# Kernel tuning notes

Measured on AMD Instinct MI355X. Metric: run time of the kernel, lower is better.

The kernel has to match this reference:

```python
import jax, jax.numpy as jnp
import numpy as np

DIM = 2048
NUM_SLOTS = 64
MEM_DIM = 512
TEMP = 0.1


def setup_inputs() -> dict:
    key = jax.random.key(0)
    k_x, k_mem, k_kp, k_vp, k_gw, k_gb = jax.random.split(key, 6)
    B, L = 8, 4096
    return {
        "x": jax.random.normal(k_x, (B, L, DIM), dtype=jnp.float32),
        "memory": jax.random.normal(k_mem, (NUM_SLOTS, MEM_DIM), dtype=jnp.float32),
        # torch Linear weight layout: [out_features, in_features]
        "key_w": jax.random.normal(k_kp, (MEM_DIM, DIM), dtype=jnp.float32) * (1.0 / np.sqrt(DIM)),
        "value_w": jax.random.normal(k_vp, (DIM, MEM_DIM), dtype=jnp.float32) * (1.0 / np.sqrt(MEM_DIM)),
        "gate_w": jax.random.normal(k_gw, (1, 2 * DIM), dtype=jnp.float32) * (1.0 / np.sqrt(2 * DIM)),
        "gate_b": jnp.zeros((1,), dtype=jnp.float32),
    }


def reference(x, memory, key_w, value_w, gate_w, gate_b):
    # query = key_proj(x): [B,L,mem_dim]
    query = jnp.einsum('bld,md->blm', x, key_w)
    # attention over memory slots: [B,L,num_slots]
    attn = jax.nn.softmax(jnp.einsum('blm,nm->bln', query, memory) / TEMP, axis=-1)
    # retrieve and project back to dim: [B,L,dim]
    retrieved = jnp.einsum('bln,nm->blm', attn, memory)
    retrieved = jnp.einsum('blm,dm->bld', retrieved, value_w)
    # gate from concat([x, retrieved]) -> Linear(2*dim, 1) -> sigmoid
    gate_logit = (jnp.einsum('bld,od->blo', x, gate_w[:, :DIM])
                  + jnp.einsum('bld,od->blo', retrieved, gate_w[:, DIM:])
                  + gate_b)
    gate = jax.nn.sigmoid(gate_logit)  # [B,L,1]
    return gate * x + (1.0 - gate) * retrieved
```

## Files before the change

kernel.cpp:

```cpp
#include <hip/hip_runtime.h>
#include <stdint.h>

#define DIM   2048
#define NSLOT 64
#define MDIM  512
#define TINV  10.0f

typedef __attribute__((ext_vector_type(4))) float     f32x4;
typedef __attribute__((ext_vector_type(8))) _Float16  half8;
typedef __attribute__((ext_vector_type(4))) unsigned int u32x4;

#define MFMA16(a,b,c) __builtin_amdgcn_mfma_f32_16x16x32_f16((a),(b),(c),0,0,0)

#define OFF_W2H   0
#define OFF_W2L   327680
#define OFF_W3T   655360
#define OFF_H     917504
#define OFF_TPART 917760


__global__ __launch_bounds__(256) void prep_w2(
    const float* __restrict__ memory, const float* __restrict__ key_w,
    const float* __restrict__ gate_w, _Float16* __restrict__ W2h,
    _Float16* __restrict__ W2l)
{
    const int tid = threadIdx.x;
    const int c = blockIdx.x;
    const int g = blockIdx.y;
    const int k = c * 256 + tid;

    if (g == 8) {
        float v = gate_w[k];
        _Float16 ph = (_Float16)v;
        _Float16 pl = (_Float16)(v - (float)ph);
        W2h[(size_t)64 * DIM + k] = ph;
        W2l[(size_t)64 * DIM + k] = pl;
        for (int r = 65; r < 80; ++r) {
            W2h[(size_t)r * DIM + k] = (_Float16)0.f;
            W2l[(size_t)r * DIM + k] = (_Float16)0.f;
        }
        return;
    }

    __shared__ __align__(16) float mem_s[8 * MDIM];
    for (int i = tid; i < 8 * MDIM; i += 256)
        mem_s[i] = memory[g * 8 * MDIM + i];
    __syncthreads();

    const f32x4* ms4 = (const f32x4*)mem_s;
    float acc[8] = {};
    for (int m4 = 0; m4 < MDIM / 4; ++m4) {
        const float kw0 = key_w[(size_t)(m4 * 4 + 0) * DIM + k];
        const float kw1 = key_w[(size_t)(m4 * 4 + 1) * DIM + k];
        const float kw2 = key_w[(size_t)(m4 * 4 + 2) * DIM + k];
        const float kw3 = key_w[(size_t)(m4 * 4 + 3) * DIM + k];
        #pragma unroll
        for (int i = 0; i < 8; ++i) {
            const f32x4 mv = ms4[i * (MDIM / 4) + m4];
            acc[i] = fmaf(mv.x, kw0, acc[i]);
            acc[i] = fmaf(mv.y, kw1, acc[i]);
            acc[i] = fmaf(mv.z, kw2, acc[i]);
            acc[i] = fmaf(mv.w, kw3, acc[i]);
        }
    }
    #pragma unroll
    for (int i = 0; i < 8; ++i) {
        float v = acc[i];
        _Float16 ph = (_Float16)v;
        _Float16 pl = (_Float16)(v - (float)ph);
        W2h[(size_t)(g * 8 + i) * DIM + k] = ph;
        W2l[(size_t)(g * 8 + i) * DIM + k] = pl;
    }
}

__global__ __launch_bounds__(256) void prep_w3t(
    const float* __restrict__ memory, const float* __restrict__ value_w,
    _Float16* __restrict__ W3T)
{
    const int tid = threadIdx.x;
    const int c = blockIdx.x;
    const int g = blockIdx.y;
    const int d = c * 256 + tid;

    __shared__ __align__(16) float mem_s[8 * MDIM];
    for (int i = tid; i < 8 * MDIM; i += 256)
        mem_s[i] = memory[g * 8 * MDIM + i];
    __syncthreads();

    const f32x4* ms4 = (const f32x4*)mem_s;
    const f32x4* vp = (const f32x4*)(value_w + (size_t)d * MDIM);
    float acc[8] = {};
    for (int m4 = 0; m4 < MDIM / 4; ++m4) {
        const f32x4 v = vp[m4];
        #pragma unroll
        for (int i = 0; i < 8; ++i) {
            const f32x4 mv = ms4[i * (MDIM / 4) + m4];
            acc[i] = fmaf(mv.x, v.x, acc[i]);
            acc[i] = fmaf(mv.y, v.y, acc[i]);
            acc[i] = fmaf(mv.z, v.z, acc[i]);
            acc[i] = fmaf(mv.w, v.w, acc[i]);
        }
    }
    #pragma unroll
    for (int i = 0; i < 8; ++i)
        W3T[(size_t)d * NSLOT + g * 8 + i] = (_Float16)acc[i];
}

__global__ __launch_bounds__(256) void prep_t(
    const float* __restrict__ value_w, const float* __restrict__ gate_w,
    float* __restrict__ tpart)
{
    const int b = blockIdx.x;
    const int tid = threadIdx.x;
    float a0 = 0.f, a1 = 0.f;
    for (int d = b * 256; d < b * 256 + 256; ++d) {
        const float gv = gate_w[DIM + d];
        a0 = fmaf(value_w[(size_t)d * MDIM + tid], gv, a0);
        a1 = fmaf(value_w[(size_t)d * MDIM + tid + 256], gv, a1);
    }
    tpart[b * 512 + tid] = a0;
    tpart[b * 512 + tid + 256] = a1;
}

__global__ __launch_bounds__(512) void prep_h(
    const float* __restrict__ memory, const float* __restrict__ tpart,
    float* __restrict__ h)
{
    __shared__ float ts[512];
    const int tid = threadIdx.x;
    float s = 0.f;
    #pragma unroll
    for (int b = 0; b < 8; ++b) s += tpart[b * 512 + tid];
    ts[tid] = s;
    __syncthreads();
    const int lane = tid & 63, w = tid >> 6;
    #pragma unroll
    for (int q = 0; q < 8; ++q) {
        const int n = w * 8 + q;
        float p = 0.f;
        for (int m = lane; m < MDIM; m += 64)
            p = fmaf(memory[(size_t)n * MDIM + m], ts[m], p);
        #pragma unroll
        for (int off = 32; off; off >>= 1) p += __shfl_xor(p, off);
        if (lane == 0) h[n] = p;
    }
}


__global__ __launch_bounds__(256) void fused_kernel(
    const float* __restrict__ x,
    const _Float16* __restrict__ W2h, const _Float16* __restrict__ W2l,
    const _Float16* __restrict__ W3T,
    const float* __restrict__ h, const float* __restrict__ gate_b,
    float* __restrict__ out)
{
    __shared__ __align__(16) _Float16 w2s[2 * 80 * 128];
    __shared__ __align__(16) _Float16 attn_s[4][16][72];
    __shared__ float gate_s[4][16];

    const int tid  = threadIdx.x;
    const int lane = tid & 63;
    const int w    = tid >> 6;
    const int arow = lane & 15;
    const int kg   = lane >> 4;
    const size_t row0 = (size_t)blockIdx.x * 64;

    f32x4 acc[5];
    {   f32x4 z = {0.f, 0.f, 0.f, 0.f};
        #pragma unroll
        for (int t = 0; t < 5; ++t) acc[t] = z; }

    const float* xrow = x + (row0 + w * 16 + arow) * DIM + kg * 8;

    u32x4 st[10];
    auto load_st = [&](int chn) {
        #pragma unroll
        for (int i = 0; i < 10; ++i) {
            const int lvl = (i >= 5) ? 1 : 0;
            const int gg = tid + i * 256 - lvl * 1280;
            const int rr = gg >> 4, gk = gg & 15;
            const _Float16* src = (lvl ? W2l : W2h) + (size_t)rr * DIM + chn * 128 + gk * 8;
            st[i] = *(const u32x4*)src;
        }
    };
    auto write_st = [&]() {
        #pragma unroll
        for (int i = 0; i < 10; ++i) {
            const int lvl = (i >= 5) ? 1 : 0;
            const int gg = tid + i * 256 - lvl * 1280;
            const int rr = gg >> 4, gk = gg & 15;
            *(u32x4*)(w2s + lvl * 10240 + rr * 128 + ((gk ^ (rr & 7)) * 8)) = st[i];
        }
    };
    f32x4 xA[8], xB[8];
    auto load_x = [&](f32x4* XB, int chn) {
        #pragma unroll
        for (int ks = 0; ks < 4; ++ks) {
            XB[ks * 2]     = *(const f32x4*)(xrow + chn * 128 + ks * 32);
            XB[ks * 2 + 1] = *(const f32x4*)(xrow + chn * 128 + ks * 32 + 4);
        }
    };
    auto compute_chunk = [&](const f32x4* XB) {
        const int s = arow & 7;
        #pragma unroll
        for (int ks = 0; ks < 4; ++ks) {
            const f32x4 xa = XB[ks * 2];
            const f32x4 xb = XB[ks * 2 + 1];
            const float xf[8] = {xa.x, xa.y, xa.z, xa.w, xb.x, xb.y, xb.z, xb.w};
            _Float16 hh[8], ll[8];
            #pragma unroll
            for (int u = 0; u < 8; ++u) {
                hh[u] = (_Float16)xf[u];
                ll[u] = (_Float16)(xf[u] - (float)hh[u]);
            }
            const half8 ah = {hh[0], hh[1], hh[2], hh[3], hh[4], hh[5], hh[6], hh[7]};
            const half8 al = {ll[0], ll[1], ll[2], ll[3], ll[4], ll[5], ll[6], ll[7]};
            const int Gb = ks * 4 + kg;
            #pragma unroll
            for (int t = 0; t < 5; ++t) {
                const _Float16* bp = w2s + (t * 16 + arow) * 128 + ((Gb ^ s) * 8);
                const half8 bh = *(const half8*)bp;
                const half8 bl = *(const half8*)(bp + 10240);
                acc[t] = MFMA16(ah, bh, acc[t]);
                acc[t] = MFMA16(al, bh, acc[t]);
                acc[t] = MFMA16(ah, bl, acc[t]);
            }
        }
    };

    load_st(0);
    load_x(xA, 0);
    for (int chp = 0; chp < 16; chp += 2) {
        __syncthreads();
        write_st();
        __syncthreads();
        load_st(chp + 1);
        load_x(xB, chp + 1);
        compute_chunk(xA);

        __syncthreads();
        write_st();
        __syncthreads();
        if (chp + 2 < 16) {
            load_st(chp + 2);
            load_x(xA, chp + 2);
        }
        compute_chunk(xB);
    }

    float hl[4];
    #pragma unroll
    for (int t = 0; t < 4; ++t) hl[t] = h[t * 16 + arow];
    const float gb = gate_b[0];

    #pragma unroll
    for (int j = 0; j < 4; ++j) {
        float m = fmaxf(fmaxf(acc[0][j], acc[1][j]), fmaxf(acc[2][j], acc[3][j]));
        #pragma unroll
        for (int off = 1; off < 16; off <<= 1) m = fmaxf(m, __shfl_xor(m, off));
        float p[4];
        float sum = 0.f;
        #pragma unroll
        for (int t = 0; t < 4; ++t) { p[t] = __expf((acc[t][j] - m) * TINV); sum += p[t]; }
        #pragma unroll
        for (int off = 1; off < 16; off <<= 1) sum += __shfl_xor(sum, off);
        const float inv = 1.f / sum;
        float gp = 0.f;
        #pragma unroll
        for (int t = 0; t < 4; ++t) {
            const float a = p[t] * inv;
            attn_s[w][kg * 4 + j][t * 16 + arow] = (_Float16)a;
            gp = fmaf(a, hl[t], gp);
        }
        #pragma unroll
        for (int off = 1; off < 16; off <<= 1) gp += __shfl_xor(gp, off);
        const float sg = __shfl(acc[4][j], lane & 48);
        if (arow == 0)
            gate_s[w][kg * 4 + j] = 1.f / (1.f + __expf(-(sg + gp + gb)));
    }

    const size_t rbase = row0 + w * 16;
    const half8 a0 = *(const half8*)(&attn_s[w][arow][kg * 8]);
    const half8 a1 = *(const half8*)(&attn_s[w][arow][kg * 8 + 32]);
    const float g = gate_s[w][arow];

    const size_t rowoff = (rbase + arow) * DIM + kg * 4;
    const float* xp = x + rowoff;
    float* op = out + rowoff;
    const _Float16* w3base = W3T + (size_t)arow * NSLOT + kg * 8;

    half8 qb0[4], qb1[4];
    f32x4 qx[4];
    #pragma unroll
    for (int s = 0; s < 4; ++s) {
        const _Float16* bp = w3base + (size_t)s * 16 * NSLOT;
        qb0[s] = *(const half8*)bp;
        qb1[s] = *(const half8*)(bp + 32);
        qx[s]  = *(const f32x4*)(xp + s * 16);
    }

    #pragma unroll 4
    for (int dt = 0; dt < 128; ++dt) {
        const int s = dt & 3;
        f32x4 r = {0.f, 0.f, 0.f, 0.f};
        r = MFMA16(qb0[s], a0, r);
        r = MFMA16(qb1[s], a1, r);
        const f32x4 xv = qx[s];
        int nt = dt + 4; if (nt > 127) nt = 127;
        const _Float16* bp = w3base + (size_t)nt * 16 * NSLOT;
        qb0[s] = *(const half8*)bp;
        qb1[s] = *(const half8*)(bp + 32);
        qx[s]  = *(const f32x4*)(xp + (size_t)nt * 16);
        f32x4 o;
        o.x = fmaf(g, xv.x - r.x, r.x);
        o.y = fmaf(g, xv.y - r.y, r.y);
        o.z = fmaf(g, xv.z - r.z, r.z);
        o.w = fmaf(g, xv.w - r.w, r.w);
        *(f32x4*)(op + dt * 16) = o;
    }
}


extern "C" void kernel_launch(void* const* d_in, const int* in_sizes, int n_in,
                              void* d_out, int out_size, void* d_ws, size_t ws_size,
                              hipStream_t stream) {
    (void)in_sizes; (void)n_in; (void)out_size; (void)ws_size;
    const float* x       = (const float*)d_in[0];
    const float* memory  = (const float*)d_in[1];
    const float* key_w   = (const float*)d_in[2];
    const float* value_w = (const float*)d_in[3];
    const float* gate_w  = (const float*)d_in[4];
    const float* gate_b  = (const float*)d_in[5];
    float* out = (float*)d_out;

    char* wsb = (char*)d_ws;
    _Float16* W2h  = (_Float16*)(wsb + OFF_W2H);
    _Float16* W2l  = (_Float16*)(wsb + OFF_W2L);
    _Float16* W3T  = (_Float16*)(wsb + OFF_W3T);
    float*    h    = (float*)(wsb + OFF_H);
    float*    tpt  = (float*)(wsb + OFF_TPART);

    prep_w2 <<<dim3(8, 9), 256, 0, stream>>>(memory, key_w, gate_w, W2h, W2l);
    prep_w3t<<<dim3(8, 8), 256, 0, stream>>>(memory, value_w, W3T);
    prep_t  <<<8, 256, 0, stream>>>(value_w, gate_w, tpt);
    prep_h  <<<1, 512, 0, stream>>>(memory, tpt, h);

    fused_kernel<<<512, 256, 0, stream>>>(x, W2h, W2l, W3T, h, gate_b, out);
}
```

Before: 322.5 us.

## Split K across two wave groups with 512-thread blocks and LDS partial reduction

Doubles the threads per block from 256 to 512. The first GEMM's K dimension is split between two wave groups, whose partial accumulators are combined through shared memory before softmax. The output projection is then split by column half across the two groups. The aim is more waves per CU to hide latency, since the grid has only 512 blocks, at the cost of extra barriers and an LDS reduction step.

```diff
diff --git a/kernel.cpp b/kernel.cpp
--- a/kernel.cpp
+++ b/kernel.cpp
@@ -147,7 +147,7 @@
 }
 
 
-__global__ __launch_bounds__(256) void fused_kernel(
+__global__ __launch_bounds__(512) void fused_kernel(
     const float* __restrict__ x,
     const _Float16* __restrict__ W2h, const _Float16* __restrict__ W2l,
     const _Float16* __restrict__ W3T,
@@ -161,6 +161,8 @@
     const int tid  = threadIdx.x;
     const int lane = tid & 63;
     const int w    = tid >> 6;
+    const int mt   = w & 3;
+    const int kh   = w >> 2;
     const int arow = lane & 15;
     const int kg   = lane >> 4;
     const size_t row0 = (size_t)blockIdx.x * 64;
@@ -170,42 +172,46 @@
         #pragma unroll
         for (int t = 0; t < 5; ++t) acc[t] = z; }
 
-    const float* xrow = x + (row0 + w * 16 + arow) * DIM + kg * 8;
-
-    u32x4 st[10];
+    const float* xrow = x + (row0 + mt * 16 + arow) * DIM + kg * 8;
+
+    u32x4 st[5];
     auto load_st = [&](int chn) {
         #pragma unroll
-        for (int i = 0; i < 10; ++i) {
-            const int lvl = (i >= 5) ? 1 : 0;
-            const int gg = tid + i * 256 - lvl * 1280;
-            const int rr = gg >> 4, gk = gg & 15;
+        for (int i = 0; i < 5; ++i) {
+            const int g  = tid + i * 512;
+            const int lvl = (g >= 1280) ? 1 : 0;
+            const int gl = g - lvl * 1280;
+            const int rr = gl >> 4, gk = gl & 15;
             const _Float16* src = (lvl ? W2l : W2h) + (size_t)rr * DIM + chn * 128 + gk * 8;
             st[i] = *(const u32x4*)src;
         }
     };
     auto write_st = [&]() {
         #pragma unroll
-        for (int i = 0; i < 10; ++i) {
-            const int lvl = (i >= 5) ? 1 : 0;
-            const int gg = tid + i * 256 - lvl * 1280;
-            const int rr = gg >> 4, gk = gg & 15;
+        for (int i = 0; i < 5; ++i) {
+            const int g  = tid + i * 512;
+            const int lvl = (g >= 1280) ? 1 : 0;
+            const int gl = g - lvl * 1280;
+            const int rr = gl >> 4, gk = gl & 15;
             *(u32x4*)(w2s + lvl * 10240 + rr * 128 + ((gk ^ (rr & 7)) * 8)) = st[i];
         }
     };
-    f32x4 xA[8], xB[8];
-    auto load_x = [&](f32x4* XB, int chn) {
-        #pragma unroll
-        for (int ks = 0; ks < 4; ++ks) {
-            XB[ks * 2]     = *(const f32x4*)(xrow + chn * 128 + ks * 32);
-            XB[ks * 2 + 1] = *(const f32x4*)(xrow + chn * 128 + ks * 32 + 4);
+    f32x4 xA[4], xB[4];
+    auto load_x = [&](f32x4* X, int chn) {
+        #pragma unroll
+        for (int ksi = 0; ksi < 2; ++ksi) {
+            const int ks = kh * 2 + ksi;
+            X[ksi * 2]     = *(const f32x4*)(xrow + chn * 128 + ks * 32);
+            X[ksi * 2 + 1] = *(const f32x4*)(xrow + chn * 128 + ks * 32 + 4);
         }
     };
-    auto compute_chunk = [&](const f32x4* XB) {
-        const int s = arow & 7;
-        #pragma unroll
-        for (int ks = 0; ks < 4; ++ks) {
-            const f32x4 xa = XB[ks * 2];
-            const f32x4 xb = XB[ks * 2 + 1];
+    auto compute_chunk = [&](const f32x4* X) {
+        const int sw = arow & 7;
+        #pragma unroll
+        for (int ksi = 0; ksi < 2; ++ksi) {
+            const int ks = kh * 2 + ksi;
+            const f32x4 xa = X[ksi * 2];
+            const f32x4 xb = X[ksi * 2 + 1];
             const float xf[8] = {xa.x, xa.y, xa.z, xa.w, xb.x, xb.y, xb.z, xb.w};
             _Float16 hh[8], ll[8];
             #pragma unroll
@@ -218,7 +224,7 @@
             const int Gb = ks * 4 + kg;
             #pragma unroll
             for (int t = 0; t < 5; ++t) {
-                const _Float16* bp = w2s + (t * 16 + arow) * 128 + ((Gb ^ s) * 8);
+                const _Float16* bp = w2s + (t * 16 + arow) * 128 + ((Gb ^ sw) * 8);
                 const half8 bh = *(const half8*)bp;
                 const half8 bl = *(const half8*)(bp + 10240);
                 acc[t] = MFMA16(ah, bh, acc[t]);
@@ -248,46 +254,62 @@
         compute_chunk(xB);
     }
 
-    float hl[4];
-    #pragma unroll
-    for (int t = 0; t < 4; ++t) hl[t] = h[t * 16 + arow];
-    const float gb = gate_b[0];
-
-    #pragma unroll
-    for (int j = 0; j < 4; ++j) {
-        float m = fmaxf(fmaxf(acc[0][j], acc[1][j]), fmaxf(acc[2][j], acc[3][j]));
-        #pragma unroll
-        for (int off = 1; off < 16; off <<= 1) m = fmaxf(m, __shfl_xor(m, off));
-        float p[4];
-        float sum = 0.f;
-        #pragma unroll
-        for (int t = 0; t < 4; ++t) { p[t] = __expf((acc[t][j] - m) * TINV); sum += p[t]; }
-        #pragma unroll
-        for (int off = 1; off < 16; off <<= 1) sum += __shfl_xor(sum, off);
-        const float inv = 1.f / sum;
-        float gp = 0.f;
-        #pragma unroll
-        for (int t = 0; t < 4; ++t) {
-            const float a = p[t] * inv;
-            attn_s[w][kg * 4 + j][t * 16 + arow] = (_Float16)a;
-            gp = fmaf(a, hl[t], gp);
-        }
-        #pragma unroll
-        for (int off = 1; off < 16; off <<= 1) gp += __shfl_xor(gp, off);
-        const float sg = __shfl(acc[4][j], lane & 48);
-        if (arow == 0)
-            gate_s[w][kg * 4 + j] = 1.f / (1.f + __expf(-(sg + gp + gb)));
-    }
-
-    const size_t rbase = row0 + w * 16;
-    const half8 a0 = *(const half8*)(&attn_s[w][arow][kg * 8]);
-    const half8 a1 = *(const half8*)(&attn_s[w][arow][kg * 8 + 32]);
-    const float g = gate_s[w][arow];
-
-    const size_t rowoff = (rbase + arow) * DIM + kg * 4;
+    __syncthreads();
+    float* ppart = (float*)w2s;
+    if (kh == 1) {
+        #pragma unroll
+        for (int t = 0; t < 5; ++t)
+            *(f32x4*)(ppart + (size_t)((mt * 5 + t) * 64 + lane) * 4) = acc[t];
+    }
+    __syncthreads();
+
+    if (kh == 0) {
+        #pragma unroll
+        for (int t = 0; t < 5; ++t)
+            acc[t] += *(const f32x4*)(ppart + (size_t)((mt * 5 + t) * 64 + lane) * 4);
+
+        float hl[4];
+        #pragma unroll
+        for (int t = 0; t < 4; ++t) hl[t] = h[t * 16 + arow];
+        const float gb = gate_b[0];
+
+        #pragma unroll
+        for (int j = 0; j < 4; ++j) {
+            float m = fmaxf(fmaxf(acc[0][j], acc[1][j]), fmaxf(acc[2][j], acc[3][j]));
+            #pragma unroll
+            for (int off = 1; off < 16; off <<= 1) m = fmaxf(m, __shfl_xor(m, off));
+            float p[4];
+            float sum = 0.f;
+            #pragma unroll
+            for (int t = 0; t < 4; ++t) { p[t] = __expf((acc[t][j] - m) * TINV); sum += p[t]; }
+            #pragma unroll
+            for (int off = 1; off < 16; off <<= 1) sum += __shfl_xor(sum, off);
+            const float inv = 1.f / sum;
+            float gp = 0.f;
+            #pragma unroll
+            for (int t = 0; t < 4; ++t) {
+                const float a = p[t] * inv;
+                attn_s[mt][kg * 4 + j][t * 16 + arow] = (_Float16)a;
+                gp = fmaf(a, hl[t], gp);
+            }
+            #pragma unroll
+            for (int off = 1; off < 16; off <<= 1) gp += __shfl_xor(gp, off);
+            const float sg = __shfl(acc[4][j], lane & 48);
+            if (arow == 0)
+                gate_s[mt][kg * 4 + j] = 1.f / (1.f + __expf(-(sg + gp + gb)));
+        }
+    }
+    __syncthreads();
+
+    const size_t rbase = row0 + mt * 16;
+    const half8 a0 = *(const half8*)(&attn_s[mt][arow][kg * 8]);
+    const half8 a1 = *(const half8*)(&attn_s[mt][arow][kg * 8 + 32]);
+    const float g = gate_s[mt][arow];
+
+    const size_t rowoff = (rbase + arow) * DIM + kh * 1024 + kg * 4;
     const float* xp = x + rowoff;
     float* op = out + rowoff;
-    const _Float16* w3base = W3T + (size_t)arow * NSLOT + kg * 8;
+    const _Float16* w3base = W3T + (size_t)(kh * 1024 + arow) * NSLOT + kg * 8;
 
     half8 qb0[4], qb1[4];
     f32x4 qx[4];
@@ -300,13 +322,13 @@
     }
 
     #pragma unroll 4
-    for (int dt = 0; dt < 128; ++dt) {
+    for (int dt = 0; dt < 64; ++dt) {
         const int s = dt & 3;
         f32x4 r = {0.f, 0.f, 0.f, 0.f};
         r = MFMA16(qb0[s], a0, r);
         r = MFMA16(qb1[s], a1, r);
         const f32x4 xv = qx[s];
-        int nt = dt + 4; if (nt > 127) nt = 127;
+        int nt = dt + 4; if (nt > 63) nt = 63;
         const _Float16* bp = w3base + (size_t)nt * 16 * NSLOT;
         qb0[s] = *(const half8*)bp;
         qb1[s] = *(const half8*)(bp + 32);
@@ -345,5 +367,5 @@
     prep_t  <<<8, 256, 0, stream>>>(value_w, gate_w, tpt);
     prep_h  <<<1, 512, 0, stream>>>(memory, tpt, h);
 
-    fused_kernel<<<512, 256, 0, stream>>>(x, W2h, W2l, W3T, h, gate_b, out);
-}
+    fused_kernel<<<512, 512, 0, stream>>>(x, W2h, W2l, W3T, h, gate_b, out);
+}
```

After: 326.3 us. No clear change (+1.2%).

## Pre-swizzle W2 into MFMA fragment order and read directly from global

Applied to the files above, without the earlier changes.

The prep kernel now writes the combined key/gate weight (high and low fp16 halves) in a layout matching the MFMA B-fragment order, so each lane loads its half8 directly from global memory. The fused kernel no longer stages W2 chunks through shared memory, which removes the LDS tile, the staging registers and four block barriers per chunk pair. The cost is more global/L2 traffic per wave, since each of the four waves re-reads the weights. The loads are no longer prefetched a chunk ahead, so their latency may be exposed in front of the MFMAs.

```diff
diff --git a/kernel.cpp b/kernel.cpp
--- a/kernel.cpp
+++ b/kernel.cpp
@@ -8,21 +8,24 @@
 
 typedef __attribute__((ext_vector_type(4))) float     f32x4;
 typedef __attribute__((ext_vector_type(8))) _Float16  half8;
-typedef __attribute__((ext_vector_type(4))) unsigned int u32x4;
 
 #define MFMA16(a,b,c) __builtin_amdgcn_mfma_f32_16x16x32_f16((a),(b),(c),0,0,0)
 
-#define OFF_W2H   0
-#define OFF_W2L   327680
-#define OFF_W3T   655360
-#define OFF_H     917504
-#define OFF_TPART 917760
+#define OFF_W2F   0
+#define OFF_W3T   1310720
+#define OFF_H     1572864
+#define OFF_TPART 1573120
+
+__device__ __forceinline__ size_t w2f_idx(int row, int k, int lvl) {
+    const int t  = row >> 4, ar = row & 15;
+    const int ch = k >> 7, ks = (k >> 5) & 3, kg = (k >> 3) & 3, e = k & 7;
+    return ((size_t)((((ch * 5 + t) * 4 + ks) * 2 + lvl) * 64) + kg * 16 + ar) * 8 + e;
+}
 
 
 __global__ __launch_bounds__(256) void prep_w2(
     const float* __restrict__ memory, const float* __restrict__ key_w,
-    const float* __restrict__ gate_w, _Float16* __restrict__ W2h,
-    _Float16* __restrict__ W2l)
+    const float* __restrict__ gate_w, _Float16* __restrict__ W2F)
 {
     const int tid = threadIdx.x;
     const int c = blockIdx.x;
@@ -33,11 +36,11 @@
         float v = gate_w[k];
         _Float16 ph = (_Float16)v;
         _Float16 pl = (_Float16)(v - (float)ph);
-        W2h[(size_t)64 * DIM + k] = ph;
-        W2l[(size_t)64 * DIM + k] = pl;
+        W2F[w2f_idx(64, k, 0)] = ph;
+        W2F[w2f_idx(64, k, 1)] = pl;
         for (int r = 65; r < 80; ++r) {
-            W2h[(size_t)r * DIM + k] = (_Float16)0.f;
-            W2l[(size_t)r * DIM + k] = (_Float16)0.f;
+            W2F[w2f_idx(r, k, 0)] = (_Float16)0.f;
+            W2F[w2f_idx(r, k, 1)] = (_Float16)0.f;
         }
         return;
     }
@@ -68,8 +71,8 @@
         float v = acc[i];
         _Float16 ph = (_Float16)v;
         _Float16 pl = (_Float16)(v - (float)ph);
-        W2h[(size_t)(g * 8 + i) * DIM + k] = ph;
-        W2l[(size_t)(g * 8 + i) * DIM + k] = pl;
+        W2F[w2f_idx(g * 8 + i, k, 0)] = ph;
+        W2F[w2f_idx(g * 8 + i, k, 1)] = pl;
     }
 }
 
@@ -149,12 +152,11 @@
 
 __global__ __launch_bounds__(256) void fused_kernel(
     const float* __restrict__ x,
-    const _Float16* __restrict__ W2h, const _Float16* __restrict__ W2l,
+    const _Float16* __restrict__ W2F,
     const _Float16* __restrict__ W3T,
     const float* __restrict__ h, const float* __restrict__ gate_b,
     float* __restrict__ out)
 {
-    __shared__ __align__(16) _Float16 w2s[2 * 80 * 128];
     __shared__ __align__(16) _Float16 attn_s[4][16][72];
     __shared__ float gate_s[4][16];
 
@@ -171,41 +173,21 @@
         for (int t = 0; t < 5; ++t) acc[t] = z; }
 
     const float* xrow = x + (row0 + w * 16 + arow) * DIM + kg * 8;
-
-    u32x4 st[10];
-    auto load_st = [&](int chn) {
-        #pragma unroll
-        for (int i = 0; i < 10; ++i) {
-            const int lvl = (i >= 5) ? 1 : 0;
-            const int gg = tid + i * 256 - lvl * 1280;
-            const int rr = gg >> 4, gk = gg & 15;
-            const _Float16* src = (lvl ? W2l : W2h) + (size_t)rr * DIM + chn * 128 + gk * 8;
-            st[i] = *(const u32x4*)src;
+    const _Float16* w2l8 = W2F + lane * 8;
+
+    f32x4 xA[8], xB[8];
+    auto load_x = [&](f32x4* X, int chn) {
+        #pragma unroll
+        for (int ks = 0; ks < 4; ++ks) {
+            X[ks * 2]     = *(const f32x4*)(xrow + chn * 128 + ks * 32);
+            X[ks * 2 + 1] = *(const f32x4*)(xrow + chn * 128 + ks * 32 + 4);
         }
     };
-    auto write_st = [&]() {
-        #pragma unroll
-        for (int i = 0; i < 10; ++i) {
-            const int lvl = (i >= 5) ? 1 : 0;
-            const int gg = tid + i * 256 - lvl * 1280;
-            const int rr = gg >> 4, gk = gg & 15;
-            *(u32x4*)(w2s + lvl * 10240 + rr * 128 + ((gk ^ (rr & 7)) * 8)) = st[i];
-        }
-    };
-    f32x4 xA[8], xB[8];
-    auto load_x = [&](f32x4* XB, int chn) {
+    auto compute_chunk = [&](const f32x4* X, int ch) {
         #pragma unroll
         for (int ks = 0; ks < 4; ++ks) {
-            XB[ks * 2]     = *(const f32x4*)(xrow + chn * 128 + ks * 32);
-            XB[ks * 2 + 1] = *(const f32x4*)(xrow + chn * 128 + ks * 32 + 4);
-        }
-    };
-    auto compute_chunk = [&](const f32x4* XB) {
-        const int s = arow & 7;
-        #pragma unroll
-        for (int ks = 0; ks < 4; ++ks) {
-            const f32x4 xa = XB[ks * 2];
-            const f32x4 xb = XB[ks * 2 + 1];
+            const f32x4 xa = X[ks * 2];
+            const f32x4 xb = X[ks * 2 + 1];
             const float xf[8] = {xa.x, xa.y, xa.z, xa.w, xb.x, xb.y, xb.z, xb.w};
             _Float16 hh[8], ll[8];
             #pragma unroll
@@ -215,12 +197,11 @@
             }
             const half8 ah = {hh[0], hh[1], hh[2], hh[3], hh[4], hh[5], hh[6], hh[7]};
             const half8 al = {ll[0], ll[1], ll[2], ll[3], ll[4], ll[5], ll[6], ll[7]};
-            const int Gb = ks * 4 + kg;
             #pragma unroll
             for (int t = 0; t < 5; ++t) {
-                const _Float16* bp = w2s + (t * 16 + arow) * 128 + ((Gb ^ s) * 8);
-                const half8 bh = *(const half8*)bp;
-                const half8 bl = *(const half8*)(bp + 10240);
+                const _Float16* p = w2l8 + (size_t)(((ch * 5 + t) * 4 + ks) * 2) * 512;
+                const half8 bh = *(const half8*)p;
+                const half8 bl = *(const half8*)(p + 512);
                 acc[t] = MFMA16(ah, bh, acc[t]);
                 acc[t] = MFMA16(al, bh, acc[t]);
                 acc[t] = MFMA16(ah, bl, acc[t]);
@@ -228,24 +209,12 @@
         }
     };
 
-    load_st(0);
     load_x(xA, 0);
     for (int chp = 0; chp < 16; chp += 2) {
-        __syncthreads();
-        write_st();
-        __syncthreads();
-        load_st(chp + 1);
         load_x(xB, chp + 1);
-        compute_chunk(xA);
-
-        __syncthreads();
-        write_st();
-        __syncthreads();
-        if (chp + 2 < 16) {
-            load_st(chp + 2);
-            load_x(xA, chp + 2);
-        }
-        compute_chunk(xB);
+        compute_chunk(xA, chp);
+        if (chp + 2 < 16) load_x(xA, chp + 2);
+        compute_chunk(xB, chp + 1);
     }
 
     float hl[4];
@@ -334,16 +303,15 @@
     float* out = (float*)d_out;
 
     char* wsb = (char*)d_ws;
-    _Float16* W2h  = (_Float16*)(wsb + OFF_W2H);
-    _Float16* W2l  = (_Float16*)(wsb + OFF_W2L);
-    _Float16* W3T  = (_Float16*)(wsb + OFF_W3T);
-    float*    h    = (float*)(wsb + OFF_H);
-    float*    tpt  = (float*)(wsb + OFF_TPART);
-
-    prep_w2 <<<dim3(8, 9), 256, 0, stream>>>(memory, key_w, gate_w, W2h, W2l);
+    _Float16* W2F = (_Float16*)(wsb + OFF_W2F);
+    _Float16* W3T = (_Float16*)(wsb + OFF_W3T);
+    float*    h   = (float*)(wsb + OFF_H);
+    float*    tpt = (float*)(wsb + OFF_TPART);
+
+    prep_w2 <<<dim3(8, 9), 256, 0, stream>>>(memory, key_w, gate_w, W2F);
     prep_w3t<<<dim3(8, 8), 256, 0, stream>>>(memory, value_w, W3T);
     prep_t  <<<8, 256, 0, stream>>>(value_w, gate_w, tpt);
     prep_h  <<<1, 512, 0, stream>>>(memory, tpt, h);
 
-    fused_kernel<<<512, 256, 0, stream>>>(x, W2h, W2l, W3T, h, gate_b, out);
-}
+    fused_kernel<<<512, 256, 0, stream>>>(x, W2F, W3T, h, gate_b, out);
+}
```

After: 389.4 us. 20.7% more time.
